# Kernel optimization log

Hardware: AMD Instinct MI355X
Metric: run time of the kernel (lower is better)

The kernel has to match this reference:

```python
import jax, jax.numpy as jnp
import numpy as np

N_NODES = 50000
N_EDGES = 1600000
IN_FEAT = 128
OUT_FEAT = 128
NUM_RELS = 40


def setup_inputs() -> dict:
    key = jax.random.key(0)
    ks = jax.random.split(key, 8)
    h = jax.random.normal(ks[0], (N_NODES, IN_FEAT), dtype=jnp.float32)
    # Linear(in_feat, out_feat, bias=False): weight shape [out, in]
    W = jax.random.normal(ks[1], (OUT_FEAT, IN_FEAT), dtype=jnp.float32) / np.sqrt(IN_FEAT)
    # attn_fc: Linear(2*out_feat, 1, bias=False): weight shape [1, 2*out]
    attn_w = jax.random.normal(ks[2], (1, 2 * OUT_FEAT), dtype=jnp.float32) / np.sqrt(2 * OUT_FEAT)
    # Embedding(num_rels, 1, padding_idx=0): row 0 zeroed
    rel_emb = jax.random.normal(ks[3], (NUM_RELS, 1), dtype=jnp.float32)
    rel_emb = rel_emb.at[0].set(0.0)
    stdv = 1.0 / np.sqrt(OUT_FEAT)
    bias_w = jax.random.uniform(ks[4], (OUT_FEAT,), minval=-stdv, maxval=stdv, dtype=jnp.float32)
    src = jax.random.randint(ks[5], (N_EDGES,), 0, N_NODES, dtype=jnp.int32)
    dst = jax.random.randint(ks[6], (N_EDGES,), 0, N_NODES, dtype=jnp.int32)
    etype = jax.random.randint(ks[7], (N_EDGES,), 0, NUM_RELS, dtype=jnp.int32)
    return {"h": h, "W": W, "attn_w": attn_w, "rel_emb": rel_emb,
            "bias_w": bias_w, "src": src, "dst": dst, "etype": etype}


def reference(h, W, attn_w, rel_emb, bias_w, src, dst, etype):
    n = h.shape[0]
    out_feat = W.shape[0]
    # z = weight(h)
    z = h @ W.T  # [N, out]
    # attn_fc(cat(z_src, z_dst)) = z_src @ w1 + z_dst @ w2 (decompose to per-node scores)
    w1 = attn_w[0, :out_feat]
    w2 = attn_w[0, out_feat:]
    s_src = z @ w1  # [N]
    s_dst = z @ w2  # [N]
    e = jax.nn.leaky_relu(s_src[src] + s_dst[dst], negative_slope=0.01)  # [E]
    rel_alpha = rel_emb[etype, 0]  # [E]
    # per-dst-node softmax over incoming edges (ragged mailbox softmax)
    m = jax.ops.segment_max(e, dst, num_segments=n)
    num = jnp.exp(e - m[dst])
    den = jax.ops.segment_sum(num, dst, num_segments=n)
    alpha = num / den[dst]
    # h_dst = sum_e rel_alpha_e * alpha_e * z[src_e]
    w_e = (rel_alpha * alpha)[:, None]  # [E,1]
    h_agg = jax.ops.segment_sum(w_e * z[src], dst, num_segments=n)  # [N, out]
    # RGCNLayer.forward: + bias; no BN/activation for GATLayer; dropout = eval identity
    return h_agg + bias_w
```

## Files before the change

kernel.cpp:

```cpp
#include <hip/hip_runtime.h>
#include <hip/hip_fp16.h>

#define NFEAT 128
#define NBUK_MAX 1024
#define HB 256
#define EPB_MAX 6272
#define HPAD 136

typedef __attribute__((ext_vector_type(8))) _Float16 f16x8;
typedef __attribute__((ext_vector_type(4))) float f32x4;

__global__ __launch_bounds__(256) void k_hist(const int* __restrict__ dst,
                                              const float* __restrict__ W,
                                              _Float16* __restrict__ Wh,
                                              int* __restrict__ hist,
                                              int e, int nbuk, int epb)
{
    __shared__ int lh[NBUK_MAX];
    const int b = blockIdx.x, tid = threadIdx.x;
    if (tid < 64) {
        int idx = b * 64 + tid;
        Wh[idx] = (_Float16)W[idx];
    }
    for (int k = tid; k < nbuk; k += 256) lh[k] = 0;
    __syncthreads();
    const int beg = b * epb, end = min(e, beg + epb);
    for (int i = beg + tid; i < end; i += 256)
        atomicAdd(&lh[dst[i] >> 6], 1);
    __syncthreads();
    for (int k = tid; k < nbuk; k += 256)
        hist[b * nbuk + k] = lh[k];
}

__global__ __launch_bounds__(256) void k_gemm_mfma(
    const float* __restrict__ h, const _Float16* __restrict__ Wh,
    const float* __restrict__ attn_w,
    __half* __restrict__ zh, float* __restrict__ s1, float* __restrict__ s2, int n)
{
    __shared__ _Float16 hsh[64 * HPAD];
    __shared__ _Float16 wsh[128 * HPAD];
    const int tid = threadIdx.x;
    const int wv = tid >> 6, lane = tid & 63;
    const int nodeBase = blockIdx.x * 64;

    {
        const uint4* Wv = reinterpret_cast<const uint4*>(Wh);
        for (int t = tid; t < 2048; t += 256) {
            int r = t >> 4, c8 = t & 15;
            *reinterpret_cast<uint4*>(&wsh[r * HPAD + c8 * 8]) = Wv[t];
        }
    }
    {
        const float4* h4 = reinterpret_cast<const float4*>(h);
        for (int t = tid; t < 64 * 32; t += 256) {
            int r = t >> 5, c4 = t & 31;
            int node = nodeBase + r;
            float4 v = (node < n) ? h4[(size_t)node * 32 + c4]
                                  : make_float4(0.f, 0.f, 0.f, 0.f);
            _Float16* d = &hsh[r * HPAD + c4 * 4];
            d[0] = (_Float16)v.x; d[1] = (_Float16)v.y;
            d[2] = (_Float16)v.z; d[3] = (_Float16)v.w;
        }
    }
    __syncthreads();

    const int arow = lane & 15;
    const int kgrp = lane >> 4;
    f32x4 acc[8];
#pragma unroll
    for (int t = 0; t < 8; ++t) acc[t] = (f32x4){0.f, 0.f, 0.f, 0.f};

#pragma unroll
    for (int k0 = 0; k0 < 128; k0 += 32) {
        f16x8 a = *reinterpret_cast<const f16x8*>(
            &hsh[(wv * 16 + arow) * HPAD + k0 + kgrp * 8]);
#pragma unroll
        for (int nt = 0; nt < 8; ++nt) {
            f16x8 b = *reinterpret_cast<const f16x8*>(
                &wsh[(nt * 16 + arow) * HPAD + k0 + kgrp * 8]);
            acc[nt] = __builtin_amdgcn_mfma_f32_16x16x32_f16(a, b, acc[nt], 0, 0, 0);
        }
    }

    {
        float pr1[4] = {0.f, 0.f, 0.f, 0.f}, pr2[4] = {0.f, 0.f, 0.f, 0.f};
#pragma unroll
        for (int nt = 0; nt < 8; ++nt) {
            float w1v = attn_w[nt * 16 + arow];
            float w2v = attn_w[128 + nt * 16 + arow];
#pragma unroll
            for (int r = 0; r < 4; ++r) {
                pr1[r] += acc[nt][r] * w1v;
                pr2[r] += acc[nt][r] * w2v;
            }
        }
#pragma unroll
        for (int off = 1; off < 16; off <<= 1) {
#pragma unroll
            for (int r = 0; r < 4; ++r) {
                pr1[r] += __shfl_xor(pr1[r], off);
                pr2[r] += __shfl_xor(pr2[r], off);
            }
        }
        if (arow == 0) {
#pragma unroll
            for (int r = 0; r < 4; ++r) {
                int node = nodeBase + wv * 16 + kgrp * 4 + r;
                if (node < n) { s1[node] = pr1[r]; s2[node] = pr2[r]; }
            }
        }
    }

    _Float16* zout = &hsh[wv * 16 * HPAD];
#pragma unroll
    for (int nt = 0; nt < 8; ++nt)
#pragma unroll
        for (int r = 0; r < 4; ++r)
            zout[(kgrp * 4 + r) * HPAD + nt * 16 + arow] = (_Float16)acc[nt][r];

    {
        int node = nodeBase + wv * 16 + arow;
        if (node < n) {
            const uint4* zsrc = reinterpret_cast<const uint4*>(&zout[arow * HPAD + kgrp * 32]);
            uint4* zdst = reinterpret_cast<uint4*>(zh) + (size_t)node * 16 + kgrp * 4;
            uint4 v0 = zsrc[0], v1 = zsrc[1], v2 = zsrc[2], v3 = zsrc[3];
            zdst[0] = v0; zdst[1] = v1; zdst[2] = v2; zdst[3] = v3;
        }
    }
}

__global__ __launch_bounds__(256) void k_scan_blocks(const int* __restrict__ hist,
                                                     int* __restrict__ base,
                                                     int* __restrict__ bucket_tot, int nbuk)
{
    __shared__ int wsum[4];
    const int k = blockIdx.x, tid = threadIdx.x;
    int v = hist[tid * nbuk + k];
    int lane = tid & 63, wave = tid >> 6;
    int x = v;
#pragma unroll
    for (int off = 1; off < 64; off <<= 1) {
        int t = __shfl_up(x, off);
        if (lane >= off) x += t;
    }
    if (lane == 63) wsum[wave] = x;
    __syncthreads();
    int wb = 0;
    for (int w = 0; w < wave; ++w) wb += wsum[w];
    base[tid * nbuk + k] = wb + x - v;
    if (tid == 255) bucket_tot[k] = wb + x;
}

__global__ __launch_bounds__(256) void k_sctr(
    const int* __restrict__ src, const int* __restrict__ dst, const int* __restrict__ etype,
    const int* __restrict__ base, const int* __restrict__ bucket_tot,
    int* __restrict__ bucket_base,
    unsigned int* __restrict__ bucket_store, int e, int nbuk, int epb)
{
    __shared__ unsigned int est[EPB_MAX];
    __shared__ unsigned short bkt[EPB_MAX];
    __shared__ int lcnt[NBUK_MAX];
    __shared__ int gbase[NBUK_MAX];
    __shared__ int lcur[NBUK_MAX];
    __shared__ int wsum[4];

    const int b = blockIdx.x, tid = threadIdx.x;
    const int beg = b * epb, end = min(e, beg + epb);
    const int cnt = end - beg;
    const int lane = tid & 63, wv = tid >> 6;
    const int C = (nbuk + 255) / 256;
    const int bi = tid * C;

    for (int k = tid; k < nbuk; k += 256) lcnt[k] = 0;

    {
        int vals[4];
        int s = 0;
#pragma unroll
        for (int j = 0; j < 4; ++j) {
            int v = 0;
            if (j < C) {
                int idx = bi + j;
                if (idx < nbuk) v = bucket_tot[idx];
            }
            vals[j] = v; s += v;
        }
        int x = s;
#pragma unroll
        for (int off = 1; off < 64; off <<= 1) {
            int t = __shfl_up(x, off);
            if (lane >= off) x += t;
        }
        if (lane == 63) wsum[wv] = x;
        __syncthreads();
        int wb = 0;
        for (int w = 0; w < wv; ++w) wb += wsum[w];
        int ex = wb + x - s;
#pragma unroll
        for (int j = 0; j < 4; ++j) {
            if (j < C) {
                int idx = bi + j;
                if (idx < nbuk) {
                    gbase[idx] = ex;
                    if (b == 0) bucket_base[idx] = ex;
                    ex += vals[j];
                }
            }
        }
    }
    __syncthreads();

    for (int i = beg + tid; i < end; i += 256)
        atomicAdd(&lcnt[dst[i] >> 6], 1);
    __syncthreads();

    {
        int vals[4];
        int s = 0;
#pragma unroll
        for (int j = 0; j < 4; ++j) {
            int v = 0;
            if (j < C) {
                int idx = bi + j;
                if (idx < nbuk) v = lcnt[idx];
            }
            vals[j] = v; s += v;
        }
        int x = s;
#pragma unroll
        for (int off = 1; off < 64; off <<= 1) {
            int t = __shfl_up(x, off);
            if (lane >= off) x += t;
        }
        if (lane == 63) wsum[wv] = x;
        __syncthreads();
        int wb = 0;
        for (int w = 0; w < wv; ++w) wb += wsum[w];
        int ex = wb + x - s;
#pragma unroll
        for (int j = 0; j < 4; ++j) {
            if (j < C) {
                int idx = bi + j;
                if (idx < nbuk) {
                    lcur[idx] = ex;
                    gbase[idx] = gbase[idx] + base[b * nbuk + idx] - ex;
                    ex += vals[j];
                }
            }
        }
    }
    __syncthreads();

    for (int i = beg + tid; i < end; i += 256) {
        int d = dst[i];
        int k = d >> 6;
        unsigned int word =
            (unsigned int)src[i] | ((unsigned int)etype[i] << 16) | ((unsigned int)(d & 63) << 22);
        int pos = atomicAdd(&lcur[k], 1);
        est[pos] = word;
        bkt[pos] = (unsigned short)k;
    }
    __syncthreads();

    for (int j = tid; j < cnt; j += 256)
        bucket_store[gbase[bkt[j]] + j] = est[j];
}

__global__ __launch_bounds__(256) void k_place(
    const unsigned int* __restrict__ bucket_store, const int* __restrict__ bucket_tot,
    const int* __restrict__ bucket_base,
    int* __restrict__ row_start, unsigned int* __restrict__ edge_list, int n)
{
    __shared__ int cnt64[64];
    const int b = blockIdx.x;
    const int tid = threadIdx.x;
    const int cnt = bucket_tot[b];
    const int base = bucket_base[b];

    if (tid < 64) cnt64[tid] = 0;
    __syncthreads();
    for (int j = tid; j < cnt; j += 256)
        atomicAdd(&cnt64[bucket_store[(size_t)base + j] >> 22], 1);
    __syncthreads();
    if (tid < 64) {
        int v = cnt64[tid];
        int x = v;
#pragma unroll
        for (int off = 1; off < 64; off <<= 1) {
            int t = __shfl_up(x, off);
            if (tid >= off) x += t;
        }
        int node = (b << 6) + tid;
        if (node < n) row_start[node] = base + x - v;
        cnt64[tid] = x - v;
    }
    if (tid == 0) {
        int bnd = (b << 6) + 64;
        if (bnd > n) bnd = n;
        row_start[bnd] = base + cnt;
    }
    __syncthreads();
    for (int j = tid; j < cnt; j += 256) {
        unsigned int pk = bucket_store[(size_t)base + j];
        int pos = base + atomicAdd(&cnt64[pk >> 22], 1);
        edge_list[pos] = pk & 0x3FFFFFu;
    }
}

__global__ __launch_bounds__(256) void k_aggregate(
    const __half* __restrict__ zh, const float* __restrict__ s1, const float* __restrict__ s2,
    const float* __restrict__ rel_emb, const float* __restrict__ bias,
    const int* __restrict__ row_start, const unsigned int* __restrict__ edge_list,
    float* __restrict__ out, int n)
{
    __shared__ uint2 lds_ws[4][64];
    const int wv   = threadIdx.x >> 6;
    const int lane = threadIdx.x & 63;
    const int node = blockIdx.x * 4 + wv;
    if (node >= n) return;

    const int beg = row_start[node];
    const int end = row_start[node + 1];
    const int deg = end - beg;
    const int quad = lane >> 4;
    const int q    = lane & 15;

    float acc[8];
#pragma unroll
    for (int j = 0; j < 8; ++j) acc[j] = 0.f;
    const uint4* z4 = reinterpret_cast<const uint4*>(zh);

    if (deg > 0) {
        const float s2n = s2[node];

        if (deg <= 64) {
            unsigned int pk = 0;
            float ev = -3.4e38f;
            const bool has = lane < deg;
            if (has) {
                pk = edge_list[beg + lane];
                ev = s1[pk & 0xFFFFu] + s2n;
                ev = ev > 0.f ? ev : 0.01f * ev;
            }
            float m = ev;
#pragma unroll
            for (int off = 32; off > 0; off >>= 1)
                m = fmaxf(m, __shfl_xor(m, off));
            float p = has ? __expf(ev - m) : 0.f;
            float den = p;
#pragma unroll
            for (int off = 32; off > 0; off >>= 1)
                den += __shfl_xor(den, off);
            const float inv = 1.f / den;
            const int   src_i = has ? (int)(pk & 0xFFFFu) : 0;
            const float wgt   = has ? rel_emb[pk >> 16] * p * inv : 0.f;

            int jb = 0;
            for (; jb + 16 <= deg; jb += 16) {
                const int j0 = jb + quad;
                int   sA = __shfl(src_i, j0),      sB = __shfl(src_i, j0 + 4);
                int   sC = __shfl(src_i, j0 + 8),  sD = __shfl(src_i, j0 + 12);
                float wA = __shfl(wgt, j0),        wB = __shfl(wgt, j0 + 4);
                float wC = __shfl(wgt, j0 + 8),    wD = __shfl(wgt, j0 + 12);
                uint4 vA = z4[(size_t)sA * 16 + q];
                uint4 vB = z4[(size_t)sB * 16 + q];
                uint4 vC = z4[(size_t)sC * 16 + q];
                uint4 vD = z4[(size_t)sD * 16 + q];
                const __half* hA = reinterpret_cast<const __half*>(&vA);
                const __half* hB = reinterpret_cast<const __half*>(&vB);
                const __half* hC = reinterpret_cast<const __half*>(&vC);
                const __half* hD = reinterpret_cast<const __half*>(&vD);
#pragma unroll
                for (int k2 = 0; k2 < 8; ++k2) {
                    acc[k2] += wA * __half2float(hA[k2]);
                    acc[k2] += wB * __half2float(hB[k2]);
                    acc[k2] += wC * __half2float(hC[k2]);
                    acc[k2] += wD * __half2float(hD[k2]);
                }
            }
            for (; jb < deg; jb += 4) {
                const int j = jb + quad;
                int   sj = __shfl(src_i, j);
                float wj = __shfl(wgt, j);
                uint4 zv = z4[(size_t)sj * 16 + q];
                const __half* hp = reinterpret_cast<const __half*>(&zv);
#pragma unroll
                for (int k2 = 0; k2 < 8; ++k2)
                    acc[k2] += wj * __half2float(hp[k2]);
            }
        } else {
            float mymax = -3.4e38f;
            for (int k = beg + lane; k < end; k += 64) {
                unsigned int pk = edge_list[k];
                float ev = s1[pk & 0xFFFFu] + s2n;
                ev = ev > 0.f ? ev : 0.01f * ev;
                mymax = fmaxf(mymax, ev);
            }
#pragma unroll
            for (int off = 32; off > 0; off >>= 1)
                mymax = fmaxf(mymax, __shfl_xor(mymax, off));
            float mysum = 0.f;
            for (int k = beg + lane; k < end; k += 64) {
                unsigned int pk = edge_list[k];
                float ev = s1[pk & 0xFFFFu] + s2n;
                ev = ev > 0.f ? ev : 0.01f * ev;
                mysum += __expf(ev - mymax);
            }
#pragma unroll
            for (int off = 32; off > 0; off >>= 1)
                mysum += __shfl_xor(mysum, off);
            const float inv = 1.f / mysum;

            for (int cb = beg; cb < end; cb += 64) {
                int k = cb + lane;
                if (k < end) {
                    unsigned int pk = edge_list[k];
                    int s = pk & 0xFFFFu;
                    float ev = s1[s] + s2n;
                    ev = ev > 0.f ? ev : 0.01f * ev;
                    lds_ws[wv][lane] = make_uint2((unsigned)s,
                        __float_as_uint(rel_emb[pk >> 16] * __expf(ev - mymax) * inv));
                }
                int cnt = min(64, end - cb);
#pragma unroll 2
                for (int j = quad; j < cnt; j += 4) {
                    uint2 t = lds_ws[wv][j];
                    float w = __uint_as_float(t.y);
                    uint4 zv = z4[(size_t)t.x * 16 + q];
                    const __half* hp = reinterpret_cast<const __half*>(&zv);
#pragma unroll
                    for (int k2 = 0; k2 < 8; ++k2)
                        acc[k2] += w * __half2float(hp[k2]);
                }
            }
        }
#pragma unroll
        for (int j = 0; j < 8; ++j) {
            acc[j] += __shfl_xor(acc[j], 16);
            acc[j] += __shfl_xor(acc[j], 32);
        }
    }

    if (quad == 0) {
        const float4* b4 = reinterpret_cast<const float4*>(bias);
        float4 b0 = b4[q * 2], b1 = b4[q * 2 + 1];
        float4* o4 = reinterpret_cast<float4*>(out);
        o4[(size_t)node * 32 + q * 2] =
            make_float4(acc[0] + b0.x, acc[1] + b0.y, acc[2] + b0.z, acc[3] + b0.w);
        o4[(size_t)node * 32 + q * 2 + 1] =
            make_float4(acc[4] + b1.x, acc[5] + b1.y, acc[6] + b1.z, acc[7] + b1.w);
    }
}

extern "C" void kernel_launch(void* const* d_in, const int* in_sizes, int n_in,
                              void* d_out, int out_size, void* d_ws, size_t ws_size,
                              hipStream_t stream) {
    const float* h      = (const float*)d_in[0];
    const float* W      = (const float*)d_in[1];
    const float* attn_w = (const float*)d_in[2];
    const float* rel    = (const float*)d_in[3];
    const float* bias   = (const float*)d_in[4];
    const int*   src    = (const int*)d_in[5];
    const int*   dst    = (const int*)d_in[6];
    const int*   etype  = (const int*)d_in[7];
    const int n = in_sizes[0] / NFEAT;
    const int e = in_sizes[5];
    const int nbuk = (n + 63) / 64;
    const int epb = (e + HB - 1) / HB;
    float* out = (float*)d_out;

    char* p = (char*)d_ws;
    __half* zh = (__half*)p;               p += (size_t)n * NFEAT * 2;
    float* s1 = (float*)p;                 p += (size_t)n * 4;
    float* s2 = (float*)p;                 p += (size_t)n * 4;
    _Float16* Wh = (_Float16*)p;           p += (size_t)NFEAT * NFEAT * 2;
    int* row_start = (int*)p;              p += (size_t)(n + 1) * 4;
    int* hist       = (int*)p;             p += (size_t)HB * nbuk * 4;
    int* base       = (int*)p;             p += (size_t)HB * nbuk * 4;
    int* bucket_tot = (int*)p;             p += (size_t)nbuk * 4;
    int* bucket_base= (int*)p;             p += (size_t)nbuk * 4;
    unsigned int* edge_list    = (unsigned int*)p;  p += (size_t)e * 4;
    unsigned int* bucket_store = (unsigned int*)p;  p += (size_t)e * 4;

    k_hist<<<HB, 256, 0, stream>>>(dst, W, Wh, hist, e, nbuk, epb);
    k_gemm_mfma<<<(n + 63) / 64, 256, 0, stream>>>(h, Wh, attn_w, zh, s1, s2, n);
    k_scan_blocks<<<nbuk, 256, 0, stream>>>(hist, base, bucket_tot, nbuk);
    k_sctr<<<HB, 256, 0, stream>>>(src, dst, etype, base, bucket_tot, bucket_base,
                                   bucket_store, e, nbuk, epb);
    k_place<<<nbuk, 256, 0, stream>>>(bucket_store, bucket_tot, bucket_base,
                                      row_start, edge_list, n);
    k_aggregate<<<(n + 3) / 4, 256, 0, stream>>>(zh, s1, s2, rel, bias, row_start, edge_list, out, n);
}
```

Before: 120.9 us.

## Fuse histogram into GEMM launch and software-pipeline aggregation gathers

Merges the dst histogram kernel and the z=hW^T MFMA GEMM into one launch, using extra blocks for histogramming, so the two run concurrently and one launch plus the W fp16 conversion buffer go away. Each GEMM block now converts W from fp32 itself, which adds redundant global reads and conversion work per block. The aggregation loop for low-degree nodes is software-pipelined so the next four z gathers are issued before the FMAs on the current ones. It also uses 32-bit byte-offset addressing and explicit fmaf.

```diff
diff --git a/kernel.cpp b/kernel.cpp
--- a/kernel.cpp
+++ b/kernel.cpp
@@ -10,44 +10,53 @@
 typedef __attribute__((ext_vector_type(8))) _Float16 f16x8;
 typedef __attribute__((ext_vector_type(4))) float f32x4;
 
-__global__ __launch_bounds__(256) void k_hist(const int* __restrict__ dst,
-                                              const float* __restrict__ W,
-                                              _Float16* __restrict__ Wh,
-                                              int* __restrict__ hist,
-                                              int e, int nbuk, int epb)
+__device__ __forceinline__ uint4 ldz(const char* zb, int s, unsigned qoff) {
+    return *reinterpret_cast<const uint4*>(zb + (((unsigned)s << 8) | qoff));
+}
+__device__ __forceinline__ void fma8(float* acc, const uint4& v, float w) {
+    const __half* hp = reinterpret_cast<const __half*>(&v);
+#pragma unroll
+    for (int k2 = 0; k2 < 8; ++k2)
+        acc[k2] = fmaf(w, __half2float(hp[k2]), acc[k2]);
+}
+
+__global__ __launch_bounds__(256) void k_fused_a(
+    const float* __restrict__ h, const float* __restrict__ W,
+    const float* __restrict__ attn_w,
+    __half* __restrict__ zh, float* __restrict__ s1, float* __restrict__ s2, int n,
+    const int* __restrict__ dst, int* __restrict__ hist, int e, int nbuk, int epb,
+    int gemmBlocks)
 {
-    __shared__ int lh[NBUK_MAX];
-    const int b = blockIdx.x, tid = threadIdx.x;
-    if (tid < 64) {
-        int idx = b * 64 + tid;
-        Wh[idx] = (_Float16)W[idx];
-    }
-    for (int k = tid; k < nbuk; k += 256) lh[k] = 0;
-    __syncthreads();
-    const int beg = b * epb, end = min(e, beg + epb);
-    for (int i = beg + tid; i < end; i += 256)
-        atomicAdd(&lh[dst[i] >> 6], 1);
-    __syncthreads();
-    for (int k = tid; k < nbuk; k += 256)
-        hist[b * nbuk + k] = lh[k];
-}
-
-__global__ __launch_bounds__(256) void k_gemm_mfma(
-    const float* __restrict__ h, const _Float16* __restrict__ Wh,
-    const float* __restrict__ attn_w,
-    __half* __restrict__ zh, float* __restrict__ s1, float* __restrict__ s2, int n)
-{
-    __shared__ _Float16 hsh[64 * HPAD];
-    __shared__ _Float16 wsh[128 * HPAD];
+    __shared__ _Float16 smem[192 * HPAD];
     const int tid = threadIdx.x;
+
+    if (blockIdx.x >= gemmBlocks) {
+        int* lh = reinterpret_cast<int*>(smem);
+        const int b = blockIdx.x - gemmBlocks;
+        for (int k = tid; k < nbuk; k += 256) lh[k] = 0;
+        __syncthreads();
+        const int beg = b * epb, end = min(e, beg + epb);
+        for (int i = beg + tid; i < end; i += 256)
+            atomicAdd(&lh[dst[i] >> 6], 1);
+        __syncthreads();
+        for (int k = tid; k < nbuk; k += 256)
+            hist[b * nbuk + k] = lh[k];
+        return;
+    }
+
+    _Float16* hsh = smem;
+    _Float16* wsh = smem + 64 * HPAD;
     const int wv = tid >> 6, lane = tid & 63;
     const int nodeBase = blockIdx.x * 64;
 
     {
-        const uint4* Wv = reinterpret_cast<const uint4*>(Wh);
-        for (int t = tid; t < 2048; t += 256) {
-            int r = t >> 4, c8 = t & 15;
-            *reinterpret_cast<uint4*>(&wsh[r * HPAD + c8 * 8]) = Wv[t];
+        const float4* W4 = reinterpret_cast<const float4*>(W);
+        for (int t = tid; t < 128 * 32; t += 256) {
+            int r = t >> 5, c4 = t & 31;
+            float4 v = W4[t];
+            _Float16* d = &wsh[r * HPAD + c4 * 4];
+            d[0] = (_Float16)v.x; d[1] = (_Float16)v.y;
+            d[2] = (_Float16)v.z; d[3] = (_Float16)v.w;
         }
     }
     {
@@ -324,11 +333,12 @@
     const int deg = end - beg;
     const int quad = lane >> 4;
     const int q    = lane & 15;
+    const unsigned qoff = (unsigned)q << 4;
+    const char* zb = reinterpret_cast<const char*>(zh);
 
     float acc[8];
 #pragma unroll
     for (int j = 0; j < 8; ++j) acc[j] = 0.f;
-    const uint4* z4 = reinterpret_cast<const uint4*>(zh);
 
     if (deg > 0) {
         const float s2n = s2[node];
@@ -356,37 +366,37 @@
             const float wgt   = has ? rel_emb[pk >> 16] * p * inv : 0.f;
 
             int jb = 0;
-            for (; jb + 16 <= deg; jb += 16) {
-                const int j0 = jb + quad;
+            if (deg >= 16) {
+                int j0 = quad;
                 int   sA = __shfl(src_i, j0),      sB = __shfl(src_i, j0 + 4);
                 int   sC = __shfl(src_i, j0 + 8),  sD = __shfl(src_i, j0 + 12);
                 float wA = __shfl(wgt, j0),        wB = __shfl(wgt, j0 + 4);
                 float wC = __shfl(wgt, j0 + 8),    wD = __shfl(wgt, j0 + 12);
-                uint4 vA = z4[(size_t)sA * 16 + q];
-                uint4 vB = z4[(size_t)sB * 16 + q];
-                uint4 vC = z4[(size_t)sC * 16 + q];
-                uint4 vD = z4[(size_t)sD * 16 + q];
-                const __half* hA = reinterpret_cast<const __half*>(&vA);
-                const __half* hB = reinterpret_cast<const __half*>(&vB);
-                const __half* hC = reinterpret_cast<const __half*>(&vC);
-                const __half* hD = reinterpret_cast<const __half*>(&vD);
-#pragma unroll
-                for (int k2 = 0; k2 < 8; ++k2) {
-                    acc[k2] += wA * __half2float(hA[k2]);
-                    acc[k2] += wB * __half2float(hB[k2]);
-                    acc[k2] += wC * __half2float(hC[k2]);
-                    acc[k2] += wD * __half2float(hD[k2]);
+                uint4 vA = ldz(zb, sA, qoff), vB = ldz(zb, sB, qoff);
+                uint4 vC = ldz(zb, sC, qoff), vD = ldz(zb, sD, qoff);
+                for (; jb + 32 <= deg; jb += 16) {
+                    int j1 = jb + 16 + quad;
+                    int   tA = __shfl(src_i, j1),      tB = __shfl(src_i, j1 + 4);
+                    int   tC = __shfl(src_i, j1 + 8),  tD = __shfl(src_i, j1 + 12);
+                    float xA = __shfl(wgt, j1),        xB = __shfl(wgt, j1 + 4);
+                    float xC = __shfl(wgt, j1 + 8),    xD = __shfl(wgt, j1 + 12);
+                    uint4 uA = ldz(zb, tA, qoff), uB = ldz(zb, tB, qoff);
+                    uint4 uC = ldz(zb, tC, qoff), uD = ldz(zb, tD, qoff);
+                    fma8(acc, vA, wA); fma8(acc, vB, wB);
+                    fma8(acc, vC, wC); fma8(acc, vD, wD);
+                    vA = uA; vB = uB; vC = uC; vD = uD;
+                    wA = xA; wB = xB; wC = xC; wD = xD;
                 }
+                fma8(acc, vA, wA); fma8(acc, vB, wB);
+                fma8(acc, vC, wC); fma8(acc, vD, wD);
+                jb += 16;
             }
             for (; jb < deg; jb += 4) {
                 const int j = jb + quad;
                 int   sj = __shfl(src_i, j);
                 float wj = __shfl(wgt, j);
-                uint4 zv = z4[(size_t)sj * 16 + q];
-                const __half* hp = reinterpret_cast<const __half*>(&zv);
-#pragma unroll
-                for (int k2 = 0; k2 < 8; ++k2)
-                    acc[k2] += wj * __half2float(hp[k2]);
+                uint4 zv = ldz(zb, sj, qoff);
+                fma8(acc, zv, wj);
             }
         } else {
             float mymax = -3.4e38f;
@@ -426,11 +436,8 @@
                 for (int j = quad; j < cnt; j += 4) {
                     uint2 t = lds_ws[wv][j];
                     float w = __uint_as_float(t.y);
-                    uint4 zv = z4[(size_t)t.x * 16 + q];
-                    const __half* hp = reinterpret_cast<const __half*>(&zv);
-#pragma unroll
-                    for (int k2 = 0; k2 < 8; ++k2)
-                        acc[k2] += w * __half2float(hp[k2]);
+                    uint4 zv = ldz(zb, (int)t.x, qoff);
+                    fma8(acc, zv, w);
                 }
             }
         }
@@ -467,13 +474,13 @@
     const int e = in_sizes[5];
     const int nbuk = (n + 63) / 64;
     const int epb = (e + HB - 1) / HB;
+    const int gemmBlocks = (n + 63) / 64;
     float* out = (float*)d_out;
 
     char* p = (char*)d_ws;
     __half* zh = (__half*)p;               p += (size_t)n * NFEAT * 2;
     float* s1 = (float*)p;                 p += (size_t)n * 4;
     float* s2 = (float*)p;                 p += (size_t)n * 4;
-    _Float16* Wh = (_Float16*)p;           p += (size_t)NFEAT * NFEAT * 2;
     int* row_start = (int*)p;              p += (size_t)(n + 1) * 4;
     int* hist       = (int*)p;             p += (size_t)HB * nbuk * 4;
     int* base       = (int*)p;             p += (size_t)HB * nbuk * 4;
@@ -482,8 +489,8 @@
     unsigned int* edge_list    = (unsigned int*)p;  p += (size_t)e * 4;
     unsigned int* bucket_store = (unsigned int*)p;  p += (size_t)e * 4;
 
-    k_hist<<<HB, 256, 0, stream>>>(dst, W, Wh, hist, e, nbuk, epb);
-    k_gemm_mfma<<<(n + 63) / 64, 256, 0, stream>>>(h, Wh, attn_w, zh, s1, s2, n);
+    k_fused_a<<<gemmBlocks + HB, 256, 0, stream>>>(h, W, attn_w, zh, s1, s2, n,
+                                                   dst, hist, e, nbuk, epb, gemmBlocks);
     k_scan_blocks<<<nbuk, 256, 0, stream>>>(hist, base, bucket_tot, nbuk);
     k_sctr<<<HB, 256, 0, stream>>>(src, dst, etype, base, bucket_tot, bucket_base,
                                    bucket_store, e, nbuk, epb);
```

New measurement: 118.2 us. -2.2%, faster.
